# Optimization experiments

Hardware: AMD Instinct MI355X
Metric: run time of the kernel (lower is better)

The kernel has to match this reference:

```python
import jax, jax.numpy as jnp
import numpy as np

VOCAB = 100000
EMB = 100
HID = 100
CTX_LEN = 60          # must equal MAX_DESC_LEN for linear_1 to fit
FACT_LEN = 20
DESC_LEN = 60


def setup_inputs() -> dict:
    key = jax.random.key(0)
    ks = jax.random.split(key, 12)
    s = 0.05
    context = jax.random.randint(ks[0], (CTX_LEN, FACT_LEN), 1, VOCAB)
    fact_lengths = jax.random.randint(ks[1], (CTX_LEN,), 1, FACT_LEN)
    description = jax.random.randint(ks[2], (DESC_LEN,), 1, VOCAB)
    emb_ctx = jax.random.normal(ks[3], (VOCAB, EMB), jnp.float32) * s
    emb_ctx = emb_ctx.at[0].set(0.0)  # padding_idx=0
    emb_dec = jax.random.normal(ks[4], (VOCAB, EMB), jnp.float32) * s
    emb_dec = emb_dec.at[0].set(0.0)
    w1 = jax.random.normal(ks[5], (HID, CTX_LEN * HID), jnp.float32) * s
    b1 = jax.random.normal(ks[6], (HID,), jnp.float32) * s
    w_ih = jax.random.normal(ks[7], (3 * HID, EMB), jnp.float32) * s
    w_hh = jax.random.normal(ks[8], (3 * HID, HID), jnp.float32) * s
    b_ih = jax.random.normal(ks[9], (3 * HID,), jnp.float32) * s
    b_hh = jax.random.normal(ks[10], (3 * HID,), jnp.float32) * s
    w_out = jax.random.normal(ks[11], (VOCAB, HID), jnp.float32) * s
    b_out = jnp.zeros((VOCAB,), jnp.float32)
    return {"context": context, "fact_lengths": fact_lengths, "description": description,
            "emb_ctx": emb_ctx, "emb_dec": emb_dec, "w1": w1, "b1": b1,
            "w_ih": w_ih, "w_hh": w_hh, "b_ih": b_ih, "b_hh": b_hh,
            "w_out": w_out, "b_out": b_out}


def _forward(context, description, emb_ctx, emb_dec, w1, b1,
             w_ih, w_hh, b_ih, b_hh, w_out, b_out):
    # ---- InputModule: embed + positional fact encoder ----
    emb = emb_ctx[context]                       # [CTX_LEN, FACT_LEN, EMB]
    slen, elen = FACT_LEN, EMB
    s = jnp.arange(slen, dtype=jnp.float32) / (slen - 1)   # [slen]
    e = jnp.arange(elen, dtype=jnp.float32) / (elen - 1)   # [elen]
    l = 1.0 - s[:, None] - e[None, :] * (1.0 - 2.0 * s[:, None])  # [slen, elen]
    facts = jnp.sum(emb * l[None], axis=1)       # [CTX_LEN, EMB]

    # ---- initial decoder hidden from flattened facts ----
    h0 = facts.reshape(1, -1) @ w1.T + b1        # [1, HID]

    x0 = emb_dec[1][None, :]                     # SOS token embedding [1, EMB]

    def step(carry, tok):
        h, x = carry
        gi = x @ w_ih.T + b_ih                   # [1, 3H]
        gh = h @ w_hh.T + b_hh
        i_r, i_z, i_n = jnp.split(gi, 3, axis=-1)
        h_r, h_z, h_n = jnp.split(gh, 3, axis=-1)
        r = jax.nn.sigmoid(i_r + h_r)
        z = jax.nn.sigmoid(i_z + h_z)
        n = jnp.tanh(i_n + r * h_n)
        h_new = (1.0 - z) * n + z * h            # [1, HID]
        logits = h_new @ w_out.T + b_out         # [1, VOCAB]
        logp = jax.nn.log_softmax(logits, axis=-1)
        loss_t = -logp[0, tok]                   # NLLLoss, batch 1
        x_next = emb_dec[tok][None, :]           # teacher forcing
        return (h_new, x_next), loss_t

    (_, _), losses = jax.lax.scan(step, (h0, x0), description)
    return jnp.sum(losses).reshape(1)            # matches torch FloatTensor([.])


def reference(context, fact_lengths, description, emb_ctx, emb_dec, w1, b1,
              w_ih, w_hh, b_ih, b_hh, w_out, b_out):
    # fact_lengths is unused by the original forward (PositionalFactEncoder ignores it)
    return _forward(context, description, emb_ctx, emb_dec, w1, b1,
                    w_ih, w_hh, b_ih, b_hh, w_out, b_out)
```

## Files before the change

### kernel.cpp

```cpp
#include <hip/hip_runtime.h>
#include <hip/hip_bf16.h>
#include <math.h>

#define VOCAB 100000
#define EMB 100
#define HID 100
#define CTX_LEN 60
#define FACT_LEN 20
#define DESC_LEN 60
#define NCHUNK (VOCAB / 16)
#define GRID_B 224
#define NWAVES_C (GRID_B * 4)
#define CPW 7

#define WS_FLAG  0
#define WS_H0    64
#define WS_GI    192
#define WS_H     18192
#define WS_MS    24256

typedef __attribute__((ext_vector_type(8))) short short8;
typedef __attribute__((ext_vector_type(4))) float f32x4;

static __device__ __forceinline__ unsigned short f2bf(float f) {
    union { float f; unsigned u; } x; x.f = f;
    unsigned r = (x.u + 0x7FFFu + ((x.u >> 16) & 1u)) >> 16;
    return (unsigned short)r;
}

static __device__ __forceinline__ void release_flag(float* ws) {
    __builtin_amdgcn_fence(__ATOMIC_RELEASE, "agent");
    __hip_atomic_store((unsigned*)ws + WS_FLAG, 1u, __ATOMIC_RELAXED, __HIP_MEMORY_SCOPE_AGENT);
}
static __device__ __forceinline__ void wait_flag(const float* ws) {
    while (__hip_atomic_load((const unsigned*)ws + WS_FLAG, __ATOMIC_RELAXED,
                             __HIP_MEMORY_SCOPE_AGENT) == 0u)
        __builtin_amdgcn_s_sleep(16);
    __builtin_amdgcn_fence(__ATOMIC_ACQUIRE, "agent");
}

__global__ __launch_bounds__(320) void kA(const int* __restrict__ context,
                                          const int* __restrict__ desc,
                                          const float* __restrict__ emb_ctx,
                                          const float* __restrict__ emb_dec,
                                          const float* __restrict__ w1,
                                          const float* __restrict__ b1,
                                          const float* __restrict__ w_ih,
                                          const float* __restrict__ b_ih,
                                          float* __restrict__ ws,
                                          float* __restrict__ out) {
    const int b = blockIdx.x, tid = threadIdx.x;
    if (b < 100) {
        __shared__ int toks[1200];
        __shared__ float facts[6000];
        __shared__ float red[320];
        for (int i = tid; i < 1200; i += 320) toks[i] = context[i];
        __syncthreads();
        for (int idx = tid; idx < 6000; idx += 320) {
            int fb = idx / 100, e = idx - fb * 100;
            float ef = e * (1.f / 99.f);
            float acc = 0.f;
            #pragma unroll
            for (int s = 0; s < 20; s++) {
                float sf = s * (1.f / 19.f);
                float l = 1.f - sf - ef * (1.f - 2.f * sf);
                acc = fmaf(emb_ctx[toks[fb * 20 + s] * 100 + e], l, acc);
            }
            facts[idx] = acc;
        }
        __syncthreads();
        const float* wr = w1 + b * 6000;
        float p = 0.f;
        for (int k = tid; k < 6000; k += 320) p = fmaf(facts[k], wr[k], p);
        red[tid] = p; __syncthreads();
        if (tid < 64) red[tid] += red[256 + tid];
        __syncthreads();
        for (int st = 128; st > 0; st >>= 1) {
            if (tid < st) red[tid] += red[tid + st];
            __syncthreads();
        }
        if (tid == 0) ws[WS_H0 + b] = red[0] + b1[b];
    } else {
        const int t = b - 100;
        const int tok = (t == 0) ? 1 : desc[t - 1];
        __shared__ float xs[100];
        if (tid < 100) xs[tid] = emb_dec[tok * 100 + tid];
        __syncthreads();
        if (tid < 300) {
            float p = b_ih[tid];
            const float* wr = w_ih + tid * 100;
            #pragma unroll 4
            for (int k = 0; k < 100; k++) p = fmaf(wr[k], xs[k], p);
            ws[WS_GI + t * 300 + tid] = p;
        }
        if (b == 100 && tid == 318) ((unsigned*)ws)[WS_FLAG] = 0u;
        if (b == 100 && tid == 319) out[0] = 0.f;
    }
}

__global__ __launch_bounds__(256, 1) void kB(const float* __restrict__ w_hh,
                                             const float* __restrict__ b_hh,
                                             const float* __restrict__ w_out,
                                             const float* __restrict__ b_out,
                                             float* __restrict__ ws) {
    __shared__ __align__(16) float smem[24128];
    const int b = blockIdx.x, tid = threadIdx.x;
    const int lane = tid & 63, wave = tid >> 6;
    const int q = lane >> 4, n = lane & 15;
    const int gw = b * 4 + wave;

    short8 bw[CPW][4];

    if (b != 0) {
        #pragma unroll
        for (int k = 0; k < CPW; k++) {
            int c = gw + k * NWAVES_C;
            if (c < NCHUNK) {
                const float* wr = w_out + (c * 16 + n) * 100;
                #pragma unroll
                for (int kt = 0; kt < 4; kt++) {
                    int k0 = kt * 32 + q * 8;
                    float va[8];
                    #pragma unroll
                    for (int jj = 0; jj < 8; jj++) va[jj] = 0.f;
                    if (k0 + 4 <= 100) {
                        float4 a = *(const float4*)(wr + k0);
                        va[0] = a.x; va[1] = a.y; va[2] = a.z; va[3] = a.w;
                    }
                    if (k0 + 8 <= 100) {
                        float4 a = *(const float4*)(wr + k0 + 4);
                        va[4] = a.x; va[5] = a.y; va[6] = a.z; va[7] = a.w;
                    }
                    short8 f;
                    #pragma unroll
                    for (int jj = 0; jj < 8; jj++) f[jj] = (short)f2bf(va[jj]);
                    bw[k][kt] = f;
                }
            }
        }
        if (tid == 0) wait_flag(ws);
        __syncthreads();
    } else {
        float* gi_lds = smem;
        float* H_lds  = smem + 18000;
        unsigned short (*h_bf)[128] = (unsigned short (*)[128])(smem + 24000);
        const int L = lane & 31;
        const int j = wave * 32 + L;
        const bool gate_lane = (lane < 32) && (j < 100);

        short8 bfr[3][2][4];
        #pragma unroll
        for (int s = 0; s < 3; s++) {
            #pragma unroll
            for (int c = 0; c < 2; c++) {
                const int jrow = wave * 32 + c * 16 + n;
                const float* wr = w_hh + (s * 100 + jrow) * 100;
                #pragma unroll
                for (int kt = 0; kt < 4; kt++) {
                    int k0 = kt * 32 + q * 8;
                    float va[8];
                    #pragma unroll
                    for (int jj = 0; jj < 8; jj++) va[jj] = 0.f;
                    if (jrow < 100) {
                        if (k0 + 4 <= 100) {
                            float4 a = *(const float4*)(wr + k0);
                            va[0] = a.x; va[1] = a.y; va[2] = a.z; va[3] = a.w;
                        }
                        if (k0 + 8 <= 100) {
                            float4 a = *(const float4*)(wr + k0 + 4);
                            va[4] = a.x; va[5] = a.y; va[6] = a.z; va[7] = a.w;
                        }
                    }
                    short8 f;
                    #pragma unroll
                    for (int jj = 0; jj < 8; jj++) f[jj] = (short)f2bf(va[jj]);
                    bfr[s][c][kt] = f;
                }
            }
        }

        {
            const float4* src = (const float4*)(ws + WS_GI);
            float4* dst = (float4*)gi_lds;
            for (int k = tid; k < 4500; k += 256) dst[k] = src[k];
        }

        float hreg = 0.f, bh0 = 0.f, bh1 = 0.f, bh2 = 0.f;
        if (gate_lane) {
            hreg = ws[WS_H0 + j];
            bh0 = b_hh[j]; bh1 = b_hh[100 + j]; bh2 = b_hh[200 + j];
        }
        if (tid < 128) {
            h_bf[0][tid] = (tid < 100) ? f2bf(ws[WS_H0 + tid]) : (unsigned short)0;
            h_bf[1][tid] = 0;
        }
        __syncthreads();

        const int js = (j < 100) ? j : 0;
        for (int t = 0; t < 60; t++) {
            const int rb = t & 1;
            float gir = gi_lds[t * 300 + js];
            float giz = gi_lds[t * 300 + 100 + js];
            float gin = gi_lds[t * 300 + 200 + js];

            short8 afr[4];
            #pragma unroll
            for (int kt = 0; kt < 4; kt++)
                afr[kt] = *(const short8*)&h_bf[rb][kt * 32 + q * 8];

            f32x4 acc[3][2];
            #pragma unroll
            for (int s = 0; s < 3; s++) {
                #pragma unroll
                for (int c = 0; c < 2; c++) {
                    f32x4 a = {0.f, 0.f, 0.f, 0.f};
                    a = __builtin_amdgcn_mfma_f32_16x16x32_bf16(afr[0], bfr[s][c][0], a, 0, 0, 0);
                    a = __builtin_amdgcn_mfma_f32_16x16x32_bf16(afr[1], bfr[s][c][1], a, 0, 0, 0);
                    a = __builtin_amdgcn_mfma_f32_16x16x32_bf16(afr[2], bfr[s][c][2], a, 0, 0, 0);
                    a = __builtin_amdgcn_mfma_f32_16x16x32_bf16(afr[3], bfr[s][c][3], a, 0, 0, 0);
                    acc[s][c] = a;
                }
            }

            if (gate_lane) {
                const int cc = L >> 4;
                float ghr = (cc ? acc[0][1][0] : acc[0][0][0]) + bh0;
                float ghz = (cc ? acc[1][1][0] : acc[1][0][0]) + bh1;
                float ghn = (cc ? acc[2][1][0] : acc[2][0][0]) + bh2;
                float r = 1.f / (1.f + __expf(-(gir + ghr)));
                float z = 1.f / (1.f + __expf(-(giz + ghz)));
                float a2 = fmaf(r, ghn, gin);
                float tt = __expf(-2.f * fabsf(a2));
                float nn = copysignf((1.f - tt) / (1.f + tt), a2);
                hreg = (1.f - z) * nn + z * hreg;
                h_bf[rb ^ 1][j] = f2bf(hreg);
                H_lds[t * 100 + j] = hreg;
            }
            __syncthreads();
        }

        {
            const float4* src = (const float4*)H_lds;
            float4* dst = (float4*)(ws + WS_H);
            for (int k = tid; k < 1500; k += 256) dst[k] = src[k];
        }
        __syncthreads();
        if (tid == 0) release_flag(ws);

        #pragma unroll
        for (int k = 0; k < CPW; k++) {
            int c = gw + k * NWAVES_C;
            if (c < NCHUNK) {
                const float* wr = w_out + (c * 16 + n) * 100;
                #pragma unroll
                for (int kt = 0; kt < 4; kt++) {
                    int k0 = kt * 32 + q * 8;
                    float va[8];
                    #pragma unroll
                    for (int jj = 0; jj < 8; jj++) va[jj] = 0.f;
                    if (k0 + 4 <= 100) {
                        float4 a = *(const float4*)(wr + k0);
                        va[0] = a.x; va[1] = a.y; va[2] = a.z; va[3] = a.w;
                    }
                    if (k0 + 8 <= 100) {
                        float4 a = *(const float4*)(wr + k0 + 4);
                        va[4] = a.x; va[5] = a.y; va[6] = a.z; va[7] = a.w;
                    }
                    short8 f;
                    #pragma unroll
                    for (int jj = 0; jj < 8; jj++) f[jj] = (short)f2bf(va[jj]);
                    bw[k][kt] = f;
                }
            }
        }
    }

    {
        const float* H = ws + WS_H;
        float* ms = ws + WS_MS;
        const int k_base = q * 8;

        short8 afr[4][4];
        #pragma unroll
        for (int mt = 0; mt < 4; mt++) {
            int m = mt * 16 + n;
            #pragma unroll
            for (int kt = 0; kt < 4; kt++) {
                int k0 = kt * 32 + k_base;
                float va[8];
                #pragma unroll
                for (int jj = 0; jj < 8; jj++) va[jj] = 0.f;
                if (m < 60) {
                    if (k0 + 4 <= 100) {
                        float4 a = *(const float4*)(H + m * 100 + k0);
                        va[0] = a.x; va[1] = a.y; va[2] = a.z; va[3] = a.w;
                    }
                    if (k0 + 8 <= 100) {
                        float4 a = *(const float4*)(H + m * 100 + k0 + 4);
                        va[4] = a.x; va[5] = a.y; va[6] = a.z; va[7] = a.w;
                    }
                }
                short8 f;
                #pragma unroll
                for (int jj = 0; jj < 8; jj++) f[jj] = (short)f2bf(va[jj]);
                afr[mt][kt] = f;
            }
        }

        float mS[16], sS[16];
        #pragma unroll
        for (int i = 0; i < 16; i++) { mS[i] = -3.0e38f; sS[i] = 0.f; }

        #pragma unroll
        for (int k = 0; k < CPW; k++) {
            int c = gw + k * NWAVES_C;
            if (c < NCHUNK) {
                int row = c * 16 + n;
                float bo = b_out[row];
                #pragma unroll
                for (int mt = 0; mt < 4; mt++) {
                    f32x4 acc = {0.f, 0.f, 0.f, 0.f};
                    acc = __builtin_amdgcn_mfma_f32_16x16x32_bf16(afr[mt][0], bw[k][0], acc, 0, 0, 0);
                    acc = __builtin_amdgcn_mfma_f32_16x16x32_bf16(afr[mt][1], bw[k][1], acc, 0, 0, 0);
                    acc = __builtin_amdgcn_mfma_f32_16x16x32_bf16(afr[mt][2], bw[k][2], acc, 0, 0, 0);
                    acc = __builtin_amdgcn_mfma_f32_16x16x32_bf16(afr[mt][3], bw[k][3], acc, 0, 0, 0);
                    #pragma unroll
                    for (int reg = 0; reg < 4; reg++) {
                        float x = acc[reg] + bo;
                        int i = mt * 4 + reg;
                        float mo = mS[i];
                        float mn = fmaxf(mo, x);
                        sS[i] = sS[i] * __expf(mo - mn) + __expf(x - mn);
                        mS[i] = mn;
                    }
                }
            }
        }

        #pragma unroll
        for (int i = 0; i < 16; i++) {
            float m = mS[i], s = sS[i];
            #pragma unroll
            for (int off = 1; off < 16; off <<= 1) {
                float m2 = __shfl_xor(m, off);
                float s2 = __shfl_xor(s, off);
                float mn = fmaxf(m, m2);
                s = s * __expf(m - mn) + s2 * __expf(m2 - mn);
                m = mn;
            }
            mS[i] = m; sS[i] = s;
        }
        if (n == 0) {
            #pragma unroll
            for (int mt = 0; mt < 4; mt++) {
                #pragma unroll
                for (int reg = 0; reg < 4; reg++) {
                    int t = mt * 16 + q * 4 + reg;
                    int i = mt * 4 + reg;
                    if (t < 60) {
                        float2 val; val.x = mS[i]; val.y = sS[i];
                        ((float2*)ms)[t * NWAVES_C + gw] = val;
                    }
                }
            }
        }
    }
}

__global__ __launch_bounds__(256) void kD(const int* __restrict__ desc,
                                          const float* __restrict__ w_out,
                                          const float* __restrict__ b_out,
                                          const float* __restrict__ ws,
                                          float* __restrict__ out) {
    const int t = blockIdx.x, tid = threadIdx.x;
    __shared__ float sm[256], ss[256], sd[256];
    const float2* msp = (const float2*)(ws + WS_MS);
    float m = -3.0e38f, s = 0.f;
    for (int i = tid; i < NWAVES_C; i += 256) {
        float2 p2 = msp[t * NWAVES_C + i];
        float mn = fmaxf(m, p2.x);
        s = s * __expf(m - mn) + p2.y * __expf(p2.x - mn);
        m = mn;
    }
    sm[tid] = m; ss[tid] = s; __syncthreads();
    for (int st = 128; st > 0; st >>= 1) {
        if (tid < st) {
            float mo = sm[tid], so = ss[tid];
            float m2 = sm[tid + st], s2 = ss[tid + st];
            float mn = fmaxf(mo, m2);
            sm[tid] = mn;
            ss[tid] = so * __expf(mo - mn) + s2 * __expf(m2 - mn);
        }
        __syncthreads();
    }
    const int tok = desc[t];
    float p = 0.f;
    if (tid < 100) p = ws[WS_H + t * 100 + tid] * w_out[tok * 100 + tid];
    sd[tid] = p; __syncthreads();
    for (int st = 128; st > 0; st >>= 1) {
        if (tid < st) sd[tid] += sd[tid + st];
        __syncthreads();
    }
    if (tid == 0) {
        float logit = sd[0] + b_out[tok];
        atomicAdd(out, sm[0] + logf(ss[0]) - logit);
    }
}

extern "C" void kernel_launch(void* const* d_in, const int* in_sizes, int n_in,
                              void* d_out, int out_size, void* d_ws, size_t ws_size,
                              hipStream_t stream) {
    const int*   context = (const int*)d_in[0];
    const int*   desc    = (const int*)d_in[2];
    const float* emb_ctx = (const float*)d_in[3];
    const float* emb_dec = (const float*)d_in[4];
    const float* w1      = (const float*)d_in[5];
    const float* b1      = (const float*)d_in[6];
    const float* w_ih    = (const float*)d_in[7];
    const float* w_hh    = (const float*)d_in[8];
    const float* b_ih    = (const float*)d_in[9];
    const float* b_hh    = (const float*)d_in[10];
    const float* w_out   = (const float*)d_in[11];
    const float* b_out   = (const float*)d_in[12];
    float* out = (float*)d_out;
    float* ws  = (float*)d_ws;

    kA<<<160, 320, 0, stream>>>(context, desc, emb_ctx, emb_dec, w1, b1, w_ih, b_ih, ws, out);
    kB<<<GRID_B, 256, 0, stream>>>(w_hh, b_hh, w_out, b_out, ws);
    kD<<<60, 256, 0, stream>>>(desc, w_out, b_out, ws, out);
}
```

Baseline: 206.2 us.

## Pipeline GRU recurrence with vocab projection via per-16-step release flags

Block 0 now runs only the GRU recurrence, writing each hidden state straight to global memory and raising one of four flags after each group of 16 timesteps. The other 223 blocks (892 waves, 8 chunks each) wait per flag and run the output-projection MFMA and online log-sum-exp for that group of rows. This lets the vocab projection overlap the serial recurrence instead of starting only after all 60 steps finish. Block 0 no longer handles vocab chunks itself, so the other blocks take on extra chunks and more register pressure, and there are extra synchronisation points.

```diff
diff --git a/kernel.cpp b/kernel.cpp
--- a/kernel.cpp
+++ b/kernel.cpp
@@ -10,10 +10,9 @@
 #define DESC_LEN 60
 #define NCHUNK (VOCAB / 16)
 #define GRID_B 224
-#define NWAVES_C (GRID_B * 4)
-#define CPW 7
-
-#define WS_FLAG  0
+#define NWAVES_T 892
+#define CPW 8
+
 #define WS_H0    64
 #define WS_GI    192
 #define WS_H     18192
@@ -28,12 +27,12 @@
     return (unsigned short)r;
 }
 
-static __device__ __forceinline__ void release_flag(float* ws) {
+static __device__ __forceinline__ void release_flag(float* ws, int idx) {
     __builtin_amdgcn_fence(__ATOMIC_RELEASE, "agent");
-    __hip_atomic_store((unsigned*)ws + WS_FLAG, 1u, __ATOMIC_RELAXED, __HIP_MEMORY_SCOPE_AGENT);
-}
-static __device__ __forceinline__ void wait_flag(const float* ws) {
-    while (__hip_atomic_load((const unsigned*)ws + WS_FLAG, __ATOMIC_RELAXED,
+    __hip_atomic_store((unsigned*)ws + idx, 1u, __ATOMIC_RELAXED, __HIP_MEMORY_SCOPE_AGENT);
+}
+static __device__ __forceinline__ void wait_flag(const float* ws, int idx) {
+    while (__hip_atomic_load((const unsigned*)ws + idx, __ATOMIC_RELAXED,
                              __HIP_MEMORY_SCOPE_AGENT) == 0u)
         __builtin_amdgcn_s_sleep(16);
     __builtin_amdgcn_fence(__ATOMIC_ACQUIRE, "agent");
@@ -93,8 +92,10 @@
             for (int k = 0; k < 100; k++) p = fmaf(wr[k], xs[k], p);
             ws[WS_GI + t * 300 + tid] = p;
         }
-        if (b == 100 && tid == 318) ((unsigned*)ws)[WS_FLAG] = 0u;
-        if (b == 100 && tid == 319) out[0] = 0.f;
+        if (b == 100) {
+            if (tid >= 304 && tid < 308) ((unsigned*)ws)[(tid - 304) * 16] = 0u;
+            if (tid == 319) out[0] = 0.f;
+        }
     }
 }
 
@@ -103,47 +104,14 @@
                                              const float* __restrict__ w_out,
                                              const float* __restrict__ b_out,
                                              float* __restrict__ ws) {
-    __shared__ __align__(16) float smem[24128];
+    __shared__ __align__(16) float smem[18128];
     const int b = blockIdx.x, tid = threadIdx.x;
     const int lane = tid & 63, wave = tid >> 6;
     const int q = lane >> 4, n = lane & 15;
-    const int gw = b * 4 + wave;
-
-    short8 bw[CPW][4];
-
-    if (b != 0) {
-        #pragma unroll
-        for (int k = 0; k < CPW; k++) {
-            int c = gw + k * NWAVES_C;
-            if (c < NCHUNK) {
-                const float* wr = w_out + (c * 16 + n) * 100;
-                #pragma unroll
-                for (int kt = 0; kt < 4; kt++) {
-                    int k0 = kt * 32 + q * 8;
-                    float va[8];
-                    #pragma unroll
-                    for (int jj = 0; jj < 8; jj++) va[jj] = 0.f;
-                    if (k0 + 4 <= 100) {
-                        float4 a = *(const float4*)(wr + k0);
-                        va[0] = a.x; va[1] = a.y; va[2] = a.z; va[3] = a.w;
-                    }
-                    if (k0 + 8 <= 100) {
-                        float4 a = *(const float4*)(wr + k0 + 4);
-                        va[4] = a.x; va[5] = a.y; va[6] = a.z; va[7] = a.w;
-                    }
-                    short8 f;
-                    #pragma unroll
-                    for (int jj = 0; jj < 8; jj++) f[jj] = (short)f2bf(va[jj]);
-                    bw[k][kt] = f;
-                }
-            }
-        }
-        if (tid == 0) wait_flag(ws);
-        __syncthreads();
-    } else {
+
+    if (b == 0) {
         float* gi_lds = smem;
-        float* H_lds  = smem + 18000;
-        unsigned short (*h_bf)[128] = (unsigned short (*)[128])(smem + 24000);
+        unsigned short (*h_bf)[128] = (unsigned short (*)[128])(smem + 18000);
         const int L = lane & 31;
         const int j = wave * 32 + L;
         const bool gate_lane = (lane < 32) && (j < 100);
@@ -234,133 +202,128 @@
                 float nn = copysignf((1.f - tt) / (1.f + tt), a2);
                 hreg = (1.f - z) * nn + z * hreg;
                 h_bf[rb ^ 1][j] = f2bf(hreg);
-                H_lds[t * 100 + j] = hreg;
+                ws[WS_H + t * 100 + j] = hreg;
             }
             __syncthreads();
-        }
-
-        {
-            const float4* src = (const float4*)H_lds;
-            float4* dst = (float4*)(ws + WS_H);
-            for (int k = tid; k < 1500; k += 256) dst[k] = src[k];
-        }
-        __syncthreads();
-        if (tid == 0) release_flag(ws);
+            if (t == 15 || t == 31 || t == 47 || t == 59) {
+                if (tid == 0) release_flag(ws, (t >> 4) * 16);
+            }
+        }
+        return;
+    }
+
+    const int gw = (b - 1) * 4 + wave;
+    short8 bw[CPW][4];
+    #pragma unroll
+    for (int k = 0; k < CPW; k++) {
+        int c = gw + k * NWAVES_T;
+        if (c < NCHUNK) {
+            const float* wr = w_out + (c * 16 + n) * 100;
+            #pragma unroll
+            for (int kt = 0; kt < 4; kt++) {
+                int k0 = kt * 32 + q * 8;
+                float va[8];
+                #pragma unroll
+                for (int jj = 0; jj < 8; jj++) va[jj] = 0.f;
+                if (k0 + 4 <= 100) {
+                    float4 a = *(const float4*)(wr + k0);
+                    va[0] = a.x; va[1] = a.y; va[2] = a.z; va[3] = a.w;
+                }
+                if (k0 + 8 <= 100) {
+                    float4 a = *(const float4*)(wr + k0 + 4);
+                    va[4] = a.x; va[5] = a.y; va[6] = a.z; va[7] = a.w;
+                }
+                short8 f;
+                #pragma unroll
+                for (int jj = 0; jj < 8; jj++) f[jj] = (short)f2bf(va[jj]);
+                bw[k][kt] = f;
+            }
+        }
+    }
+
+    const float* H = ws + WS_H;
+    const int k_base = q * 8;
+    float mS[16], sS[16];
+    #pragma unroll
+    for (int i = 0; i < 16; i++) { mS[i] = -3.0e38f; sS[i] = 0.f; }
+
+    #pragma unroll
+    for (int p = 0; p < 4; p++) {
+        if (tid == 0) wait_flag(ws, p * 16);
+        __syncthreads();
+
+        short8 afr[4];
+        const int m = p * 16 + n;
+        #pragma unroll
+        for (int kt = 0; kt < 4; kt++) {
+            int k0 = kt * 32 + k_base;
+            float va[8];
+            #pragma unroll
+            for (int jj = 0; jj < 8; jj++) va[jj] = 0.f;
+            if (m < 60) {
+                if (k0 + 4 <= 100) {
+                    float4 a = *(const float4*)(H + m * 100 + k0);
+                    va[0] = a.x; va[1] = a.y; va[2] = a.z; va[3] = a.w;
+                }
+                if (k0 + 8 <= 100) {
+                    float4 a = *(const float4*)(H + m * 100 + k0 + 4);
+                    va[4] = a.x; va[5] = a.y; va[6] = a.z; va[7] = a.w;
+                }
+            }
+            short8 f;
+            #pragma unroll
+            for (int jj = 0; jj < 8; jj++) f[jj] = (short)f2bf(va[jj]);
+            afr[kt] = f;
+        }
 
         #pragma unroll
         for (int k = 0; k < CPW; k++) {
-            int c = gw + k * NWAVES_C;
-            if (c < NCHUNK) {
-                const float* wr = w_out + (c * 16 + n) * 100;
-                #pragma unroll
-                for (int kt = 0; kt < 4; kt++) {
-                    int k0 = kt * 32 + q * 8;
-                    float va[8];
-                    #pragma unroll
-                    for (int jj = 0; jj < 8; jj++) va[jj] = 0.f;
-                    if (k0 + 4 <= 100) {
-                        float4 a = *(const float4*)(wr + k0);
-                        va[0] = a.x; va[1] = a.y; va[2] = a.z; va[3] = a.w;
-                    }
-                    if (k0 + 8 <= 100) {
-                        float4 a = *(const float4*)(wr + k0 + 4);
-                        va[4] = a.x; va[5] = a.y; va[6] = a.z; va[7] = a.w;
-                    }
-                    short8 f;
-                    #pragma unroll
-                    for (int jj = 0; jj < 8; jj++) f[jj] = (short)f2bf(va[jj]);
-                    bw[k][kt] = f;
-                }
-            }
-        }
-    }
-
-    {
-        const float* H = ws + WS_H;
-        float* ms = ws + WS_MS;
-        const int k_base = q * 8;
-
-        short8 afr[4][4];
-        #pragma unroll
-        for (int mt = 0; mt < 4; mt++) {
-            int m = mt * 16 + n;
-            #pragma unroll
-            for (int kt = 0; kt < 4; kt++) {
-                int k0 = kt * 32 + k_base;
-                float va[8];
-                #pragma unroll
-                for (int jj = 0; jj < 8; jj++) va[jj] = 0.f;
-                if (m < 60) {
-                    if (k0 + 4 <= 100) {
-                        float4 a = *(const float4*)(H + m * 100 + k0);
-                        va[0] = a.x; va[1] = a.y; va[2] = a.z; va[3] = a.w;
-                    }
-                    if (k0 + 8 <= 100) {
-                        float4 a = *(const float4*)(H + m * 100 + k0 + 4);
-                        va[4] = a.x; va[5] = a.y; va[6] = a.z; va[7] = a.w;
-                    }
-                }
-                short8 f;
-                #pragma unroll
-                for (int jj = 0; jj < 8; jj++) f[jj] = (short)f2bf(va[jj]);
-                afr[mt][kt] = f;
-            }
-        }
-
-        float mS[16], sS[16];
-        #pragma unroll
-        for (int i = 0; i < 16; i++) { mS[i] = -3.0e38f; sS[i] = 0.f; }
-
-        #pragma unroll
-        for (int k = 0; k < CPW; k++) {
-            int c = gw + k * NWAVES_C;
+            int c = gw + k * NWAVES_T;
             if (c < NCHUNK) {
                 int row = c * 16 + n;
                 float bo = b_out[row];
-                #pragma unroll
-                for (int mt = 0; mt < 4; mt++) {
-                    f32x4 acc = {0.f, 0.f, 0.f, 0.f};
-                    acc = __builtin_amdgcn_mfma_f32_16x16x32_bf16(afr[mt][0], bw[k][0], acc, 0, 0, 0);
-                    acc = __builtin_amdgcn_mfma_f32_16x16x32_bf16(afr[mt][1], bw[k][1], acc, 0, 0, 0);
-                    acc = __builtin_amdgcn_mfma_f32_16x16x32_bf16(afr[mt][2], bw[k][2], acc, 0, 0, 0);
-                    acc = __builtin_amdgcn_mfma_f32_16x16x32_bf16(afr[mt][3], bw[k][3], acc, 0, 0, 0);
-                    #pragma unroll
-                    for (int reg = 0; reg < 4; reg++) {
-                        float x = acc[reg] + bo;
-                        int i = mt * 4 + reg;
-                        float mo = mS[i];
-                        float mn = fmaxf(mo, x);
-                        sS[i] = sS[i] * __expf(mo - mn) + __expf(x - mn);
-                        mS[i] = mn;
-                    }
-                }
-            }
-        }
-
-        #pragma unroll
-        for (int i = 0; i < 16; i++) {
-            float m = mS[i], s = sS[i];
-            #pragma unroll
-            for (int off = 1; off < 16; off <<= 1) {
-                float m2 = __shfl_xor(m, off);
-                float s2 = __shfl_xor(s, off);
-                float mn = fmaxf(m, m2);
-                s = s * __expf(m - mn) + s2 * __expf(m2 - mn);
-                m = mn;
-            }
-            mS[i] = m; sS[i] = s;
-        }
-        if (n == 0) {
-            #pragma unroll
-            for (int mt = 0; mt < 4; mt++) {
+                f32x4 acc = {0.f, 0.f, 0.f, 0.f};
+                acc = __builtin_amdgcn_mfma_f32_16x16x32_bf16(afr[0], bw[k][0], acc, 0, 0, 0);
+                acc = __builtin_amdgcn_mfma_f32_16x16x32_bf16(afr[1], bw[k][1], acc, 0, 0, 0);
+                acc = __builtin_amdgcn_mfma_f32_16x16x32_bf16(afr[2], bw[k][2], acc, 0, 0, 0);
+                acc = __builtin_amdgcn_mfma_f32_16x16x32_bf16(afr[3], bw[k][3], acc, 0, 0, 0);
                 #pragma unroll
                 for (int reg = 0; reg < 4; reg++) {
-                    int t = mt * 16 + q * 4 + reg;
-                    int i = mt * 4 + reg;
-                    if (t < 60) {
-                        float2 val; val.x = mS[i]; val.y = sS[i];
-                        ((float2*)ms)[t * NWAVES_C + gw] = val;
-                    }
+                    float x = acc[reg] + bo;
+                    const int i = p * 4 + reg;
+                    float mo = mS[i];
+                    float mn = fmaxf(mo, x);
+                    sS[i] = sS[i] * __expf(mo - mn) + __expf(x - mn);
+                    mS[i] = mn;
+                }
+            }
+        }
+    }
+
+    #pragma unroll
+    for (int i = 0; i < 16; i++) {
+        float m = mS[i], s = sS[i];
+        #pragma unroll
+        for (int off = 1; off < 16; off <<= 1) {
+            float m2 = __shfl_xor(m, off);
+            float s2 = __shfl_xor(s, off);
+            float mn = fmaxf(m, m2);
+            s = s * __expf(m - mn) + s2 * __expf(m2 - mn);
+            m = mn;
+        }
+        mS[i] = m; sS[i] = s;
+    }
+    if (n == 0) {
+        float* ms = ws + WS_MS;
+        #pragma unroll
+        for (int mt = 0; mt < 4; mt++) {
+            #pragma unroll
+            for (int reg = 0; reg < 4; reg++) {
+                int t = mt * 16 + q * 4 + reg;
+                int i = mt * 4 + reg;
+                if (t < 60) {
+                    float2 val; val.x = mS[i]; val.y = sS[i];
+                    ((float2*)ms)[t * NWAVES_T + gw] = val;
                 }
             }
         }
@@ -376,8 +339,8 @@
     __shared__ float sm[256], ss[256], sd[256];
     const float2* msp = (const float2*)(ws + WS_MS);
     float m = -3.0e38f, s = 0.f;
-    for (int i = tid; i < NWAVES_C; i += 256) {
-        float2 p2 = msp[t * NWAVES_C + i];
+    for (int i = tid; i < NWAVES_T; i += 256) {
+        float2 p2 = msp[t * NWAVES_T + i];
         float mn = fmaxf(m, p2.x);
         s = s * __expf(m - mn) + p2.y * __expf(p2.x - mn);
         m = mn;
```

Result: faster. 201.9 us (-2.1%).
